# Kernel tuning notes

Hardware: AMD Instinct MI355X
Metric: run time of the kernel (lower is better)

The kernel has to match this reference:

```python
import jax, jax.numpy as jnp
import numpy as np

B_, L_, DIN, DM, DS, DR, K = 2, 1024, 1024, 2048, 16, 128, 4


def setup_inputs() -> dict:
    key = jax.random.key(0)
    ks = jax.random.split(key, 10)
    s = lambda k, shape, sc=0.02: (jax.random.normal(k, shape, jnp.float32) * sc)
    A_init = jnp.tile(jnp.arange(1, DS + 1, dtype=jnp.float32)[None, :], (DM, 1))  # (DM, DS)
    return {
        'x_in': jax.random.normal(ks[0], (B_, L_, DIN), jnp.float32),
        'W_in': s(ks[1], (DIN, DM)),
        'W_res': s(ks[2], (DIN, DM)),
        'W_out': s(ks[3], (DM, DIN)),
        'conv_w': s(ks[4], (DM, K), 0.1),   # depthwise conv weight (torch shape (DM,1,K) squeezed)
        'conv_b': jnp.zeros((DM,), jnp.float32),
        'A_log': jnp.log(A_init),
        'D': jnp.ones((DM,), jnp.float32),
        'W_B': s(ks[5], (DM, DS)),
        'W_C': s(ks[6], (DM, DS)),
        'W_dt': s(ks[7], (DM, DR)),
        'dt_w': s(ks[8], (DR, DM)),
        'dt_b': jnp.zeros((DM,), jnp.float32),
    }


def reference(x_in, W_in, W_res, W_out, conv_w, conv_b, A_log, D, W_B, W_C, W_dt, dt_w, dt_b):
    Bb, L, _ = x_in.shape
    x = x_in @ W_in                     # (B, L, DM)
    res = x_in @ W_res                  # (B, L, DM)
    # Causal depthwise conv1d: pad left k-1, truncate to L (matches Conv1d(padding=k-1)[:, :, :L])
    xp = jnp.pad(x, ((0, 0), (K - 1, 0), (0, 0)))
    xc = conv_b
    for i in range(K):
        xc = xc + xp[:, i:i + L, :] * conv_w[:, i]
    xc = jax.nn.silu(xc)                # (B, L, DM)
    # Selective SSM (fused_ssm)
    A = -jnp.exp(A_log)                 # (DM, DS)
    Bp = xc @ W_B                       # (B, L, DS)
    Cp = xc @ W_C                       # (B, L, DS)
    delta = jax.nn.softplus((xc @ W_dt) @ dt_w + dt_b)  # (B, L, DM)
    dA = jnp.exp(delta[..., None] * A)                       # (B, L, DM, DS)
    dBu = delta[..., None] * Bp[:, :, None, :] * xc[..., None]  # (B, L, DM, DS)

    def step(h, inp):
        dA_t, dBu_t, C_t = inp
        h = dA_t * h + dBu_t                         # (B, DM, DS)
        y = jnp.einsum('bdn,bn->bd', h, C_t)         # (B, DM)
        return h, y

    h0 = jnp.zeros((Bb, DM, DS), jnp.float32)
    _, ys = jax.lax.scan(step, h0, (dA.transpose(1, 0, 2, 3), dBu.transpose(1, 0, 2, 3), Cp.transpose(1, 0, 2)))
    y = ys.transpose(1, 0, 2) + D * xc  # (B, L, DM)
    y = y * jax.nn.silu(res)
    return y @ W_out                    # (B, L, DIN)
```

## Files before the change

kernel.cpp:

```cpp
#include <hip/hip_runtime.h>
#include <hip/hip_bf16.h>

constexpr int B_  = 2;
constexpr int L_  = 1024;
constexpr int DIN = 1024;
constexpr int DM  = 2048;
constexpr int DS  = 16;
constexpr int DR  = 128;
constexpr int KC  = 4;
constexpr int M_  = B_ * L_;
constexpr int NP2 = 256;
constexpr int NPC = 160;
constexpr int KSLICES = 8;
constexpr int KSL = DM / KSLICES;

constexpr int NC = 32;
constexpr int CL = L_ / NC;
constexpr int S_ = B_ * DM * DS;

typedef __bf16 bf16x8 __attribute__((ext_vector_type(8)));
typedef float  f32x4  __attribute__((ext_vector_type(4)));

__device__ __forceinline__ void gload_lds16(const void* g, void* l) {
    __builtin_amdgcn_global_load_lds(
        (const __attribute__((address_space(1))) void*)g,
        (__attribute__((address_space(3))) void*)l, 16, 0, 0);
}

__device__ __forceinline__ void transpose_block(const float* __restrict__ in,
                                                __bf16* __restrict__ out,
                                                int R, int C, int bx, int by, int t) {
    __shared__ float tile[32][33];
    int tx = t & 31, ty = t >> 5;
    #pragma unroll
    for (int j = 0; j < 32; j += 8)
        tile[ty + j][tx] = in[(size_t)(by * 32 + ty + j) * C + (bx * 32 + tx)];
    __syncthreads();
    #pragma unroll
    for (int j = 0; j < 32; j += 8)
        out[(size_t)(bx * 32 + ty + j) * R + (by * 32 + tx)] = (__bf16)tile[tx][ty + j];
}

__global__ void prep_all(const float* __restrict__ x_in, const float* __restrict__ W_in,
                         const float* __restrict__ W_res, const float* __restrict__ W_out,
                         const float* __restrict__ dt_w,
                         const float* __restrict__ W_B, const float* __restrict__ W_C,
                         const float* __restrict__ W_dt, const float* __restrict__ conv_w,
                         __bf16* __restrict__ xinB, __bf16* __restrict__ WinT,
                         __bf16* __restrict__ WresT, __bf16* __restrict__ WoutT,
                         __bf16* __restrict__ dtwT, __bf16* __restrict__ projW,
                         float* __restrict__ cwT) {
    int blk = blockIdx.x, t = threadIdx.x;
    if (blk < 8192) {
        int i = blk * 256 + t;
        xinB[i] = (__bf16)x_in[i];
    } else if (blk < 10240) {
        int b = blk - 8192;
        transpose_block(W_in, WinT, DIN, DM, b % 64, b / 64, t);
    } else if (blk < 12288) {
        int b = blk - 10240;
        transpose_block(W_res, WresT, DIN, DM, b % 64, b / 64, t);
    } else if (blk < 14336) {
        int b = blk - 12288;
        transpose_block(W_out, WoutT, DM, DIN, b % 32, b / 32, t);
    } else if (blk < 14592) {
        int b = blk - 14336;
        transpose_block(dt_w, dtwT, DR, DM, b % 64, b / 64, t);
    } else if (blk < 16640) {
        int i = (blk - 14592) * 256 + t;
        int k = i % DM;
        int n = i / DM;
        float v = 0.f;
        if (n < 16)        v = W_B[(size_t)k * DS + n];
        else if (n < 32)   v = W_C[(size_t)k * DS + (n - 16)];
        else if (n < 160)  v = W_dt[(size_t)k * DR + (n - 32)];
        projW[i] = (__bf16)v;
    } else {
        int j = (blk - 16640) * 256 + t;
        int tap = j / DM, d = j % DM;
        cwT[j] = conv_w[d * KC + tap];
    }
}

__global__ void reduce_split(const __bf16* __restrict__ PpartB, float* __restrict__ Bp,
                             float* __restrict__ Cp, __bf16* __restrict__ dtmpB) {
    int i = blockIdx.x * 256 + threadIdx.x;
    int row = i / NPC, c = i % NPC;
    float v = 0.f;
    #pragma unroll
    for (int ks = 0; ks < KSLICES; ks++)
        v += (float)PpartB[(size_t)ks * M_ * NPC + i];
    if (c < 16)       Bp[(size_t)row * DS + c] = v;
    else if (c < 32)  Cp[(size_t)row * DS + (c - 16)] = v;
    else              dtmpB[(size_t)row * DR + (c - 32)] = (__bf16)v;
}

template<int EPI>
__global__ void gemm_tile128(const __bf16* __restrict__ A, const __bf16* __restrict__ BT,
                             float* __restrict__ Cf, __bf16* __restrict__ Cb,
                             const float* __restrict__ bias, int M, int N, int K,
                             int lda, int ldb) {
    __shared__ __bf16 sA[128 * 32];
    __shared__ __bf16 sB[128 * 32];
    int t = threadIdx.x;
    int lane = t & 63, w = t >> 6;
    int wm = w >> 1, wn = w & 1;
    int m0 = blockIdx.y * 128, n0 = blockIdx.x * 128;
    int kbase = blockIdx.z * K;
    int q = lane >> 4, rr = lane & 15;

    f32x4 acc[4][4] = {};

    int srow = t >> 2;
    int slot = t & 3;

    for (int kt = 0; kt < K; kt += 32) {
        __syncthreads();
        #pragma unroll
        for (int rnd = 0; rnd < 2; rnd++) {
            int row = srow + rnd * 64;
            int gkb = slot ^ ((row >> 1) & 3);
            const __bf16* ga = A  + (size_t)(m0 + row) * lda + kbase + kt + gkb * 8;
            const __bf16* gb = BT + (size_t)(n0 + row) * ldb + kbase + kt + gkb * 8;
            __bf16* la = sA + rnd * 2048 + w * 512;
            __bf16* lb = sB + rnd * 2048 + w * 512;
            gload_lds16(ga, la);
            gload_lds16(gb, lb);
        }
        __syncthreads();

        bf16x8 af[4], bfr[4];
        #pragma unroll
        for (int i = 0; i < 4; i++) {
            int rowA = wm * 64 + i * 16 + rr;
            af[i] = *(const bf16x8*)(sA + rowA * 32 + ((q ^ ((rowA >> 1) & 3)) * 8));
            int rowB = wn * 64 + i * 16 + rr;
            bfr[i] = *(const bf16x8*)(sB + rowB * 32 + ((q ^ ((rowB >> 1) & 3)) * 8));
        }
        #pragma unroll
        for (int i = 0; i < 4; i++)
            #pragma unroll
            for (int j = 0; j < 4; j++)
                acc[i][j] = __builtin_amdgcn_mfma_f32_16x16x32_bf16(af[i], bfr[j], acc[i][j], 0, 0, 0);
    }

    #pragma unroll
    for (int i = 0; i < 4; i++) {
        #pragma unroll
        for (int j = 0; j < 4; j++) {
            int col = n0 + wn * 64 + j * 16 + rr;
            #pragma unroll
            for (int jj = 0; jj < 4; jj++) {
                int row = m0 + wm * 64 + i * 16 + q * 4 + jj;
                float v = acc[i][j][jj];
                if (EPI == 1) {
                    float z = v + bias[col];
                    Cb[(size_t)row * N + col] = (__bf16)((z > 20.f) ? z : log1pf(__expf(z)));
                } else if (EPI == 2) {
                    if (col < DM) ((__bf16*)Cf)[(size_t)row * DM + col] = (__bf16)v;
                    else          Cb[(size_t)row * DM + (col - DM)] = (__bf16)v;
                } else {
                    if (col < NPC)
                        Cb[(size_t)blockIdx.z * M * NPC + (size_t)row * NPC + col] = (__bf16)v;
                }
            }
        }
    }
}

__global__ void gemm_out64(const __bf16* __restrict__ A, const __bf16* __restrict__ BT,
                           float* __restrict__ C, int M, int N, int K, int lda, int ldb) {
    __shared__ __bf16 sA[128 * 32];
    __shared__ __bf16 sB[64 * 32];
    int t = threadIdx.x;
    int lane = t & 63, w = t >> 6;
    int m0 = blockIdx.y * 128, n0 = blockIdx.x * 64;
    int q = lane >> 4, rr = lane & 15;

    f32x4 acc[2][4] = {};
    int srow = t >> 2;
    int slot = t & 3;

    for (int kt = 0; kt < K; kt += 32) {
        __syncthreads();
        #pragma unroll
        for (int rnd = 0; rnd < 2; rnd++) {
            int row = srow + rnd * 64;
            int gkb = slot ^ ((row >> 1) & 3);
            const __bf16* ga = A + (size_t)(m0 + row) * lda + kt + gkb * 8;
            __bf16* la = sA + rnd * 2048 + w * 512;
            gload_lds16(ga, la);
        }
        {
            int row = srow;
            int gkb = slot ^ ((row >> 1) & 3);
            const __bf16* gb = BT + (size_t)(n0 + row) * ldb + kt + gkb * 8;
            __bf16* lb = sB + w * 512;
            gload_lds16(gb, lb);
        }
        __syncthreads();

        bf16x8 af[2], bfr[4];
        #pragma unroll
        for (int i = 0; i < 2; i++) {
            int rowA = w * 32 + i * 16 + rr;
            af[i] = *(const bf16x8*)(sA + rowA * 32 + ((q ^ ((rowA >> 1) & 3)) * 8));
        }
        #pragma unroll
        for (int j = 0; j < 4; j++) {
            int rowB = j * 16 + rr;
            bfr[j] = *(const bf16x8*)(sB + rowB * 32 + ((q ^ ((rowB >> 1) & 3)) * 8));
        }
        #pragma unroll
        for (int i = 0; i < 2; i++)
            #pragma unroll
            for (int j = 0; j < 4; j++)
                acc[i][j] = __builtin_amdgcn_mfma_f32_16x16x32_bf16(af[i], bfr[j], acc[i][j], 0, 0, 0);
    }

    #pragma unroll
    for (int i = 0; i < 2; i++) {
        #pragma unroll
        for (int j = 0; j < 4; j++) {
            int col = n0 + j * 16 + rr;
            #pragma unroll
            for (int jj = 0; jj < 4; jj++) {
                int row = m0 + w * 32 + i * 16 + q * 4 + jj;
                C[(size_t)row * N + col] = acc[i][j][jj];
            }
        }
    }
}

__global__ void conv_silu(const __bf16* __restrict__ x, const float* __restrict__ cwT,
                          const float* __restrict__ bias, __bf16* __restrict__ xcB) {
    int row = blockIdx.x;
    int d   = threadIdx.x * 8;
    int l   = row % L_;
    size_t base = (size_t)row * DM + d;

    float acc[8];
    {
        const f32x4* b4 = (const f32x4*)(bias + d);
        f32x4 b0 = b4[0], b1 = b4[1];
        #pragma unroll
        for (int q = 0; q < 4; q++) { acc[q] = b0[q]; acc[4 + q] = b1[q]; }
    }
    #pragma unroll
    for (int i = 0; i < KC; i++) {
        int li = l - (KC - 1) + i;
        if (li >= 0) {
            bf16x8 xv = *(const bf16x8*)(x + base + (size_t)(i - (KC - 1)) * DM);
            const f32x4* w4 = (const f32x4*)(cwT + (size_t)i * DM + d);
            f32x4 w0 = w4[0], w1 = w4[1];
            #pragma unroll
            for (int q = 0; q < 4; q++) {
                acc[q]     = fmaf((float)xv[q],     w0[q], acc[q]);
                acc[4 + q] = fmaf((float)xv[4 + q], w1[q], acc[4 + q]);
            }
        }
    }
    bf16x8 out;
    #pragma unroll
    for (int q = 0; q < 8; q++) {
        float v = acc[q] / (1.f + __expf(-acc[q]));
        out[q] = (__bf16)v;
    }
    *(bf16x8*)(xcB + base) = out;
}

__global__ void scan_phase1(const __bf16* __restrict__ delta, const __bf16* __restrict__ xc,
                            const float* __restrict__ Bp, const float* __restrict__ A_log,
                            __bf16* __restrict__ aprodB, __bf16* __restrict__ cendB) {
    int blk = blockIdx.x;
    int c   = blk % NC;
    int rem = blk / NC;
    int dmt = rem % (DM / 256);
    int b   = rem / (DM / 256);
    int t   = threadIdx.x;
    int dm  = dmt * 256 + t;
    int l0  = c * CL;

    __shared__ float sB[CL * DS];
    sB[t]       = Bp[((size_t)b * L_ + l0) * DS + t];
    sB[t + 256] = Bp[((size_t)b * L_ + l0) * DS + t + 256];
    __syncthreads();

    float Aval[DS];
    {
        const f32x4* Ap = (const f32x4*)(A_log + (size_t)dm * DS);
        #pragma unroll
        for (int r4 = 0; r4 < 4; r4++) {
            f32x4 a = Ap[r4];
            #pragma unroll
            for (int q = 0; q < 4; q++) Aval[r4 * 4 + q] = -__expf(a[q]);
        }
    }

    float h[DS], ap[DS];
    #pragma unroll
    for (int i = 0; i < DS; i++) { h[i] = 0.f; ap[i] = 1.f; }

    size_t base = ((size_t)b * L_ + l0) * DM + dm;
    #pragma unroll 4
    for (int j = 0; j < CL; j++) {
        float dl  = (float)delta[base + (size_t)j * DM];
        float xv  = (float)xc[base + (size_t)j * DM];
        float cmn = dl * xv;
        const f32x4* sB4 = (const f32x4*)(sB + j * DS);
        #pragma unroll
        for (int r4 = 0; r4 < 4; r4++) {
            f32x4 bv = sB4[r4];
            #pragma unroll
            for (int q = 0; q < 4; q++) {
                int i = r4 * 4 + q;
                float dA = __expf(dl * Aval[i]);
                ap[i] *= dA;
                h[i] = fmaf(dA, h[i], cmn * bv[q]);
            }
        }
    }

    size_t s = ((size_t)(b * DM + dm)) * DS;
    #pragma unroll
    for (int r8 = 0; r8 < 2; r8++) {
        bf16x8 va, vh;
        #pragma unroll
        for (int q = 0; q < 8; q++) { va[q] = (__bf16)ap[r8 * 8 + q]; vh[q] = (__bf16)h[r8 * 8 + q]; }
        ((bf16x8*)(aprodB + (size_t)c * S_ + s))[r8] = va;
        ((bf16x8*)(cendB  + (size_t)c * S_ + s))[r8] = vh;
    }
}

__global__ void scan_phase2(const __bf16* __restrict__ aprodB, const __bf16* __restrict__ cendB,
                            __bf16* __restrict__ hinitB) {
    int u8 = (blockIdx.x * 256 + threadIdx.x) * 8;
    float h[8];
    #pragma unroll
    for (int q = 0; q < 8; q++) h[q] = 0.f;
    #pragma unroll
    for (int c = 0; c < NC; c++) {
        bf16x8 a  = *(const bf16x8*)(aprodB + (size_t)c * S_ + u8);
        bf16x8 ce = *(const bf16x8*)(cendB  + (size_t)c * S_ + u8);
        bf16x8 ho;
        #pragma unroll
        for (int q = 0; q < 8; q++) {
            ho[q] = (__bf16)h[q];
            h[q] = fmaf((float)a[q], h[q], (float)ce[q]);
        }
        *(bf16x8*)(hinitB + (size_t)c * S_ + u8) = ho;
    }
}

__global__ void scan_phase3(const __bf16* __restrict__ delta, const __bf16* __restrict__ xc,
                            const float* __restrict__ Bp, const float* __restrict__ Cp,
                            const __bf16* __restrict__ res, const float* __restrict__ A_log,
                            const float* __restrict__ Dw, const __bf16* __restrict__ hinitB,
                            __bf16* __restrict__ ybar) {
    int blk = blockIdx.x;
    int c   = blk % NC;
    int rem = blk / NC;
    int dmt = rem % (DM / 256);
    int b   = rem / (DM / 256);
    int t   = threadIdx.x;
    int dm  = dmt * 256 + t;
    int l0  = c * CL;

    __shared__ float sB[CL * DS];
    __shared__ float sC[CL * DS];
    sB[t]       = Bp[((size_t)b * L_ + l0) * DS + t];
    sB[t + 256] = Bp[((size_t)b * L_ + l0) * DS + t + 256];
    sC[t]       = Cp[((size_t)b * L_ + l0) * DS + t];
    sC[t + 256] = Cp[((size_t)b * L_ + l0) * DS + t + 256];
    __syncthreads();

    float Aval[DS];
    {
        const f32x4* Ap = (const f32x4*)(A_log + (size_t)dm * DS);
        #pragma unroll
        for (int r4 = 0; r4 < 4; r4++) {
            f32x4 a = Ap[r4];
            #pragma unroll
            for (int q = 0; q < 4; q++) Aval[r4 * 4 + q] = -__expf(a[q]);
        }
    }
    float Dval = Dw[dm];

    float h[DS];
    {
        size_t s = ((size_t)(b * DM + dm)) * DS;
        #pragma unroll
        for (int r8 = 0; r8 < 2; r8++) {
            bf16x8 v = ((const bf16x8*)(hinitB + (size_t)c * S_ + s))[r8];
            #pragma unroll
            for (int q = 0; q < 8; q++) h[r8 * 8 + q] = (float)v[q];
        }
    }

    size_t base = ((size_t)b * L_ + l0) * DM + dm;
    #pragma unroll 4
    for (int j = 0; j < CL; j++) {
        float dl  = (float)delta[base + (size_t)j * DM];
        float xv  = (float)xc[base + (size_t)j * DM];
        float rv  = (float)res[base + (size_t)j * DM];
        float cmn = dl * xv;
        float y = 0.f;
        const f32x4* sB4 = (const f32x4*)(sB + j * DS);
        const f32x4* sC4 = (const f32x4*)(sC + j * DS);
        #pragma unroll
        for (int r4 = 0; r4 < 4; r4++) {
            f32x4 bv = sB4[r4];
            f32x4 cv = sC4[r4];
            #pragma unroll
            for (int q = 0; q < 4; q++) {
                int i = r4 * 4 + q;
                float dA = __expf(dl * Aval[i]);
                h[i] = fmaf(dA, h[i], cmn * bv[q]);
                y = fmaf(h[i], cv[q], y);
            }
        }
        float g = rv / (1.f + __expf(-rv));
        ybar[base + (size_t)j * DM] = (__bf16)((y + Dval * xv) * g);
    }
}

extern "C" void kernel_launch(void* const* d_in, const int* in_sizes, int n_in,
                              void* d_out, int out_size, void* d_ws, size_t ws_size,
                              hipStream_t stream) {
    const float* x_in   = (const float*)d_in[0];
    const float* W_in   = (const float*)d_in[1];
    const float* W_res  = (const float*)d_in[2];
    const float* W_out  = (const float*)d_in[3];
    const float* conv_w = (const float*)d_in[4];
    const float* conv_b = (const float*)d_in[5];
    const float* A_log  = (const float*)d_in[6];
    const float* Dw     = (const float*)d_in[7];
    const float* W_B    = (const float*)d_in[8];
    const float* W_C    = (const float*)d_in[9];
    const float* W_dt   = (const float*)d_in[10];
    const float* dt_w   = (const float*)d_in[11];
    const float* dt_b   = (const float*)d_in[12];

    float* ws_f = (float*)d_ws;
    float* Bp    = ws_f;
    float* Cp    = Bp + (size_t)M_ * DS;
    float* cwT   = Cp + (size_t)M_ * DS;
    __bf16* bf_base = (__bf16*)(cwT + (size_t)KC * DM);
    __bf16* ybar   = bf_base;
    __bf16* xinB   = ybar   + (size_t)M_ * DM;
    __bf16* WinT   = xinB   + (size_t)M_ * DIN;
    __bf16* WresT  = WinT   + (size_t)DM * DIN;
    __bf16* WoutT  = WresT  + (size_t)DM * DIN;
    __bf16* xB     = WoutT  + (size_t)DIN * DM;
    __bf16* xcB    = xB     + (size_t)M_ * DM;
    __bf16* projW  = xcB    + (size_t)M_ * DM;
    __bf16* dtwT   = projW  + (size_t)NP2 * DM;
    __bf16* dtmpB  = dtwT   + (size_t)DM * DR;
    __bf16* deltaB = dtmpB  + (size_t)M_ * DR;
    __bf16* resB   = deltaB + (size_t)M_ * DM;
    __bf16* aprodB = resB   + (size_t)M_ * DM;
    __bf16* cendB  = aprodB + (size_t)NC * S_;
    __bf16* hinitB = cendB  + (size_t)NC * S_;
    __bf16* PpartB = hinitB + (size_t)NC * S_;

    prep_all<<<16672, 256, 0, stream>>>(x_in, W_in, W_res, W_out, dt_w, W_B, W_C, W_dt,
                                        conv_w, xinB, WinT, WresT, WoutT, dtwT, projW, cwT);

    gemm_tile128<2><<<dim3((2 * DM) / 128, M_ / 128, 1), 256, 0, stream>>>(
        xinB, WinT, (float*)xB, resB, nullptr, M_, 2 * DM, DIN, DIN, DIN);

    conv_silu<<<M_, 256, 0, stream>>>(xB, cwT, conv_b, xcB);

    gemm_tile128<4><<<dim3(NP2 / 128, M_ / 128, KSLICES), 256, 0, stream>>>(
        xcB, projW, nullptr, PpartB, nullptr, M_, NP2, KSL, DM, DM);
    reduce_split<<<(M_ * NPC) / 256, 256, 0, stream>>>(PpartB, Bp, Cp, dtmpB);

    gemm_tile128<1><<<dim3(DM / 128, M_ / 128, 1), 256, 0, stream>>>(
        dtmpB, dtwT, nullptr, deltaB, dt_b, M_, DM, DR, DR, DR);

    int nblk = B_ * (DM / 256) * NC;
    scan_phase1<<<nblk, 256, 0, stream>>>(deltaB, xcB, Bp, A_log, aprodB, cendB);
    scan_phase2<<<S_ / (256 * 8), 256, 0, stream>>>(aprodB, cendB, hinitB);
    scan_phase3<<<nblk, 256, 0, stream>>>(deltaB, xcB, Bp, Cp, resB, A_log, Dw, hinitB, ybar);

    gemm_out64<<<dim3(DIN / 64, M_ / 128), 256, 0, stream>>>(
        ybar, WoutT, (float*)d_out, M_, DIN, DM, DM, DM);
}
```

Baseline: 266.0 us.

## Fold chunk-carry scan into phase3, removing the separate phase2 kernel

Removes the scan_phase2 kernel that prefix-combined per-chunk decay products and end states into initial states. Each scan_phase3 block now recomputes its own starting state by folding over all preceding chunks' aprod/cend values. This drops one kernel launch and the hinit buffer write/read, but adds redundant work: block c reads c chunks' worth of state, so total reads grow quadratically in the number of chunks. It also creates load imbalance between early and late chunks.

```diff
diff --git a/kernel.cpp b/kernel.cpp
--- a/kernel.cpp
+++ b/kernel.cpp
@@ -332,30 +332,11 @@
     }
 }
 
-__global__ void scan_phase2(const __bf16* __restrict__ aprodB, const __bf16* __restrict__ cendB,
-                            __bf16* __restrict__ hinitB) {
-    int u8 = (blockIdx.x * 256 + threadIdx.x) * 8;
-    float h[8];
-    #pragma unroll
-    for (int q = 0; q < 8; q++) h[q] = 0.f;
-    #pragma unroll
-    for (int c = 0; c < NC; c++) {
-        bf16x8 a  = *(const bf16x8*)(aprodB + (size_t)c * S_ + u8);
-        bf16x8 ce = *(const bf16x8*)(cendB  + (size_t)c * S_ + u8);
-        bf16x8 ho;
-        #pragma unroll
-        for (int q = 0; q < 8; q++) {
-            ho[q] = (__bf16)h[q];
-            h[q] = fmaf((float)a[q], h[q], (float)ce[q]);
-        }
-        *(bf16x8*)(hinitB + (size_t)c * S_ + u8) = ho;
-    }
-}
-
 __global__ void scan_phase3(const __bf16* __restrict__ delta, const __bf16* __restrict__ xc,
                             const float* __restrict__ Bp, const float* __restrict__ Cp,
                             const __bf16* __restrict__ res, const float* __restrict__ A_log,
-                            const float* __restrict__ Dw, const __bf16* __restrict__ hinitB,
+                            const float* __restrict__ Dw,
+                            const __bf16* __restrict__ aprodB, const __bf16* __restrict__ cendB,
                             __bf16* __restrict__ ybar) {
     int blk = blockIdx.x;
     int c   = blk % NC;
@@ -387,13 +368,21 @@
     float Dval = Dw[dm];
 
     float h[DS];
+    #pragma unroll
+    for (int i = 0; i < DS; i++) h[i] = 0.f;
     {
         size_t s = ((size_t)(b * DM + dm)) * DS;
-        #pragma unroll
-        for (int r8 = 0; r8 < 2; r8++) {
-            bf16x8 v = ((const bf16x8*)(hinitB + (size_t)c * S_ + s))[r8];
-            #pragma unroll
-            for (int q = 0; q < 8; q++) h[r8 * 8 + q] = (float)v[q];
+        for (int cc = 0; cc < c; cc++) {
+            #pragma unroll
+            for (int r8 = 0; r8 < 2; r8++) {
+                bf16x8 a  = ((const bf16x8*)(aprodB + (size_t)cc * S_ + s))[r8];
+                bf16x8 ce = ((const bf16x8*)(cendB  + (size_t)cc * S_ + s))[r8];
+                #pragma unroll
+                for (int q = 0; q < 8; q++) {
+                    int i = r8 * 8 + q;
+                    h[i] = fmaf((float)a[q], h[i], (float)ce[q]);
+                }
+            }
         }
     }
 
@@ -460,8 +449,7 @@
     __bf16* resB   = deltaB + (size_t)M_ * DM;
     __bf16* aprodB = resB   + (size_t)M_ * DM;
     __bf16* cendB  = aprodB + (size_t)NC * S_;
-    __bf16* hinitB = cendB  + (size_t)NC * S_;
-    __bf16* PpartB = hinitB + (size_t)NC * S_;
+    __bf16* PpartB = cendB  + (size_t)NC * S_;
 
     prep_all<<<16672, 256, 0, stream>>>(x_in, W_in, W_res, W_out, dt_w, W_B, W_C, W_dt,
                                         conv_w, xinB, WinT, WresT, WoutT, dtwT, projW, cwT);
@@ -480,8 +468,8 @@
 
     int nblk = B_ * (DM / 256) * NC;
     scan_phase1<<<nblk, 256, 0, stream>>>(deltaB, xcB, Bp, A_log, aprodB, cendB);
-    scan_phase2<<<S_ / (256 * 8), 256, 0, stream>>>(aprodB, cendB, hinitB);
-    scan_phase3<<<nblk, 256, 0, stream>>>(deltaB, xcB, Bp, Cp, resB, A_log, Dw, hinitB, ybar);
+    scan_phase3<<<nblk, 256, 0, stream>>>(deltaB, xcB, Bp, Cp, resB, A_log, Dw,
+                                          aprodB, cendB, ybar);
 
     gemm_out64<<<dim3(DIN / 64, M_ / 128), 256, 0, stream>>>(
         ybar, WoutT, (float*)d_out, M_, DIN, DM, DM, DM);
```

New measurement: 267.6 us. No clear change (+0.6%).
